# Kernel optimization log

Measured on AMD Instinct MI355X. Metric: run time of the kernel, lower is better.

Reference implementation:

```python
import jax, jax.numpy as jnp
import numpy as np

N_NODES = 50000
N_EDGES = 640000
F = 128          # feat_dims == hidden_dims == out_channels
L = 5            # num_layers of GatedGraphConv


def setup_inputs() -> dict:
    key = jax.random.key(0)
    ks = jax.random.split(key, 9)
    s = 1.0 / np.sqrt(F)
    x = jax.random.normal(ks[0], (N_NODES, F), dtype=jnp.float32)
    edge_index = jax.random.randint(ks[1], (2, N_EDGES), 0, N_NODES, dtype=jnp.int64)
    weight = jax.random.uniform(ks[2], (L, F, F), jnp.float32, -s, s)   # per-layer linear
    w_ih = jax.random.uniform(ks[3], (3 * F, F), jnp.float32, -s, s)     # GRUCell input weights
    w_hh = jax.random.uniform(ks[4], (3 * F, F), jnp.float32, -s, s)     # GRUCell hidden weights
    b_ih = jax.random.uniform(ks[5], (3 * F,), jnp.float32, -s, s)
    b_hh = jax.random.uniform(ks[6], (3 * F,), jnp.float32, -s, s)
    lin_w = jax.random.uniform(ks[7], (1, F), jnp.float32, -s, s)
    lin_b = jax.random.uniform(ks[8], (1,), jnp.float32, -s, s)
    return {"x": x, "edge_index": edge_index, "weight": weight,
            "w_ih": w_ih, "w_hh": w_hh, "b_ih": b_ih, "b_hh": b_hh,
            "lin_w": lin_w, "lin_b": lin_b}


def _gru_cell(m, h, w_ih, w_hh, b_ih, b_hh):
    gi = m @ w_ih.T + b_ih          # [N, 3F]
    gh = h @ w_hh.T + b_hh          # [N, 3F]
    i_r, i_z, i_n = jnp.split(gi, 3, axis=-1)
    h_r, h_z, h_n = jnp.split(gh, 3, axis=-1)
    r = jax.nn.sigmoid(i_r + h_r)
    z = jax.nn.sigmoid(i_z + h_z)
    n = jnp.tanh(i_n + r * h_n)
    return (1.0 - z) * n + z * h


def reference(x, edge_index, weight, w_ih, w_hh, b_ih, b_hh, lin_w, lin_b):
    src = edge_index[0]   # message source (x_j)
    dst = edge_index[1]   # aggregation target
    n_nodes = x.shape[0]
    h = x  # in_channels == out_channels, no padding needed
    for i in range(L):
        m = h @ weight[i]                                   # [N, F]
        agg = jax.ops.segment_sum(m[src], dst, num_segments=n_nodes)  # add-aggregate
        h = _gru_cell(agg, h, w_ih, w_hh, b_ih, b_hh)
    out = jax.nn.relu(h) @ lin_w.T + lin_b                  # [N, 1]
    return out
```

## Files before the change

kernel.cpp:

```cpp
#include <hip/hip_runtime.h>

typedef float f32x4 __attribute__((ext_vector_type(4)));
typedef __bf16 bf16x8 __attribute__((ext_vector_type(8)));
typedef unsigned short u16x8 __attribute__((ext_vector_type(8)));

#define F 128

__device__ __forceinline__ unsigned short bf16_rne(float f) {
  unsigned u = __float_as_uint(f);
  u += 0x7FFFu + ((u >> 16) & 1u);
  return (unsigned short)(u >> 16);
}
__device__ __forceinline__ float bf16f(unsigned short s) {
  return __uint_as_float((unsigned)s << 16);
}


__global__ void split8_kernel(const float* __restrict__ in,
                              unsigned short* __restrict__ hi, unsigned short* __restrict__ lo,
                              int N) {
  int i = blockIdx.x * 256 + threadIdx.x;
  if (i >= N * 16) return;
  int node = i >> 4, f8 = i & 15;
  const float4* p = (const float4*)(in + (size_t)node * F + f8 * 8);
  float4 a = p[0], b = p[1];
  float v[8] = {a.x, a.y, a.z, a.w, b.x, b.y, b.z, b.w};
  u16x8 vh, vl;
#pragma unroll
  for (int e = 0; e < 8; ++e) {
    unsigned short x = bf16_rne(v[e]);
    vh[e] = x;
    vl[e] = bf16_rne(v[e] - bf16f(x));
  }
  size_t o = (size_t)node * F + f8 * 8;
  *(u16x8*)(hi + o) = vh;
  *(u16x8*)(lo + o) = vl;
}

__global__ void prep_w_kernel(const float* __restrict__ W, const float* __restrict__ w_ih,
                              const float* __restrict__ w_hh,
                              unsigned short* __restrict__ Bpack, int L) {
  int idx = blockIdx.x * 256 + threadIdx.x;
  if (idx >= L * 98304) return;
  int e = idx & 7;
  int l = (idx >> 3) & 63;
  int fp = idx >> 9;
  int part = fp % 3;
  int rest = fp / 3;
  int w = rest & 7, g = (rest >> 3) & 1, ks = (rest >> 4) & 3, t = rest >> 6;
  int j = part * 128 + w * 16 + (l & 15);
  int k = ks * 32 + ((l >> 4) & 3) * 8 + e;
  float v;
  if (g == 0) {
    const float* wi = w_ih + (size_t)j * 128;
    const float* wk = W + (size_t)t * 16384 + (size_t)k * 128;
    float acc = 0.f;
#pragma unroll 4
    for (int c = 0; c < 128; ++c) acc = fmaf(wk[c], wi[c], acc);
    v = acc;
  } else {
    v = w_hh[(size_t)j * 128 + k];
  }
  int ff = ((ks * 2 + g) * 8 + w) * 3 + part;
  size_t base = (size_t)t * 196608 + (size_t)ff * 1024 + l * 8 + e;
  unsigned short x = bf16_rne(v);
  Bpack[base] = x;
  Bpack[base + 512] = bf16_rne(v - bf16f(x));
}

__global__ void hist_kernel(const int* __restrict__ ei, int* __restrict__ cnt, int E) {
  int e = blockIdx.x * 256 + threadIdx.x;
  if (e < E) atomicAdd(&cnt[ei[E + e]], 1);
}

__global__ void scan1_kernel(const int* __restrict__ cnt, int* __restrict__ exscan,
                             int* __restrict__ chunk_sums, int N) {
  __shared__ int tmp[256];
  int i = blockIdx.x * 256 + threadIdx.x;
  int v = (i < N) ? cnt[i] : 0;
  tmp[threadIdx.x] = v;
  __syncthreads();
#pragma unroll
  for (int off = 1; off < 256; off <<= 1) {
    int a = (threadIdx.x >= off) ? tmp[threadIdx.x - off] : 0;
    __syncthreads();
    tmp[threadIdx.x] += a;
    __syncthreads();
  }
  if (i < N) exscan[i] = tmp[threadIdx.x] - v;
  if (threadIdx.x == 255) chunk_sums[blockIdx.x] = tmp[255];
}

__global__ void scan2_kernel(int* __restrict__ chunk_sums, int nchunk) {
  __shared__ int tmp[256];
  int v = (threadIdx.x < nchunk) ? chunk_sums[threadIdx.x] : 0;
  tmp[threadIdx.x] = v;
  __syncthreads();
#pragma unroll
  for (int off = 1; off < 256; off <<= 1) {
    int a = (threadIdx.x >= off) ? tmp[threadIdx.x - off] : 0;
    __syncthreads();
    tmp[threadIdx.x] += a;
    __syncthreads();
  }
  if (threadIdx.x < nchunk) chunk_sums[threadIdx.x] = tmp[threadIdx.x] - v;
}

__global__ void finalize_rowptr_kernel(const int* __restrict__ exscan,
                                       const int* __restrict__ chunk_sums,
                                       int* __restrict__ rowptr, int* __restrict__ cursor,
                                       int N, int E) {
  int i = blockIdx.x * 256 + threadIdx.x;
  if (i < N) {
    int v = exscan[i] + chunk_sums[i >> 8];
    rowptr[i] = v;
    cursor[i] = v;
  }
  if (i == N) rowptr[N] = E;
}

__global__ void place_kernel(const int* __restrict__ ei, int* __restrict__ cursor,
                             int* __restrict__ csr_src, int E) {
  int e = blockIdx.x * 256 + threadIdx.x;
  if (e >= E) return;
  int pos = atomicAdd(&cursor[ei[E + e]], 1);
  csr_src[pos] = ei[e];
}

__global__ __launch_bounds__(256) void gather_kernel(
    const unsigned short* __restrict__ hh, const unsigned short* __restrict__ hl,
    const int* __restrict__ rowptr, const int* __restrict__ csr_src,
    unsigned short* __restrict__ shi, unsigned short* __restrict__ slo, int N) {
  int node = blockIdx.x * 4 + (threadIdx.x >> 6);
  if (node >= N) return;
  const int lane = threadIdx.x & 63;
  const int grp = lane >> 4, sub = lane & 15;
  const int par = grp >> 1;
  const unsigned short* base = (grp & 1) ? hl : hh;
  const int beg = rowptr[node], end = rowptr[node + 1];
  float a[8] = {0.f, 0.f, 0.f, 0.f, 0.f, 0.f, 0.f, 0.f};
  int j = beg;
  for (; j + 8 <= end; j += 8) {
    int e0 = csr_src[j + par];
    int e1 = csr_src[j + 2 + par];
    int e2 = csr_src[j + 4 + par];
    int e3 = csr_src[j + 6 + par];
    u16x8 v0 = *(const u16x8*)(base + (size_t)e0 * F + sub * 8);
    u16x8 v1 = *(const u16x8*)(base + (size_t)e1 * F + sub * 8);
    u16x8 v2 = *(const u16x8*)(base + (size_t)e2 * F + sub * 8);
    u16x8 v3 = *(const u16x8*)(base + (size_t)e3 * F + sub * 8);
#pragma unroll
    for (int q = 0; q < 8; ++q)
      a[q] += (bf16f(v0[q]) + bf16f(v1[q])) + (bf16f(v2[q]) + bf16f(v3[q]));
  }
  for (; j + 2 <= end; j += 2) {
    int e0 = csr_src[j + par];
    u16x8 v0 = *(const u16x8*)(base + (size_t)e0 * F + sub * 8);
#pragma unroll
    for (int q = 0; q < 8; ++q) a[q] += bf16f(v0[q]);
  }
  if (j < end && par == 0) {
    int e0 = csr_src[j];
    u16x8 v0 = *(const u16x8*)(base + (size_t)e0 * F + sub * 8);
#pragma unroll
    for (int q = 0; q < 8; ++q) a[q] += bf16f(v0[q]);
  }
#pragma unroll
  for (int q = 0; q < 8; ++q) {
    a[q] += __shfl_xor(a[q], 32, 64);
    a[q] += __shfl_xor(a[q], 16, 64);
  }
  if (grp == 0) {
    u16x8 o;
#pragma unroll
    for (int q = 0; q < 8; ++q) o[q] = bf16_rne(a[q]);
    *(u16x8*)(shi + (size_t)node * F + sub * 8) = o;
  } else if (grp == 1) {
    u16x8 o;
#pragma unroll
    for (int q = 0; q < 8; ++q) {
      unsigned short x = bf16_rne(a[q]);
      o[q] = bf16_rne(a[q] - bf16f(x));
    }
    *(u16x8*)(slo + (size_t)node * F + sub * 8) = o;
  }
}

__device__ __forceinline__ void g2l(const void* g, void* l) {
  __builtin_amdgcn_global_load_lds((const __attribute__((address_space(1))) void*)g,
                                   (__attribute__((address_space(3))) void*)l, 16, 0, 0);
}

#define LOADB(hs, slot)                                                          \
  {                                                                              \
    const unsigned char* bg = Bbase + (size_t)(hs) * 49152;                      \
    _Pragma("unroll") for (int i = 0; i < 6; ++i)                                \
        Bf[slot][i] = *(const bf16x8*)(bg + i * 1024);                           \
  }
#define LOADA(hs, slot)                                                          \
  {                                                                              \
    const int ks_ = (hs) >> 1, g_ = (hs) & 1;                                    \
    const unsigned char* bh = lds + ((g_ * 2) * 4 + ks_) * 4096 + lrow * 64 + kq * 16;      \
    const unsigned char* bl = lds + ((g_ * 2 + 1) * 4 + ks_) * 4096 + lrow * 64 + kq * 16;  \
    _Pragma("unroll") for (int t = 0; t < 4; ++t) {                              \
      Af[slot][t] = *(const bf16x8*)(bh + t * 1024);                             \
      Af[slot][4 + t] = *(const bf16x8*)(bl + t * 1024);                         \
    }                                                                            \
  }
#define DOMFMA(hs, slot)                                                         \
  {                                                                              \
    const int g_ = (hs) & 1;                                                     \
    __builtin_amdgcn_s_setprio(1);                                               \
    _Pragma("unroll") for (int part = 0; part < 3; ++part)                       \
        _Pragma("unroll") for (int t = 0; t < 4; ++t) {                          \
      const int ai = (t * 3 + part) * 2 + g_;                                    \
      acc[ai] = __builtin_amdgcn_mfma_f32_16x16x32_bf16(Af[slot][t], Bf[slot][part * 2], acc[ai], 0, 0, 0);     \
      acc[ai] = __builtin_amdgcn_mfma_f32_16x16x32_bf16(Af[slot][4 + t], Bf[slot][part * 2], acc[ai], 0, 0, 0); \
      acc[ai] = __builtin_amdgcn_mfma_f32_16x16x32_bf16(Af[slot][t], Bf[slot][part * 2 + 1], acc[ai], 0, 0, 0); \
    }                                                                            \
    __builtin_amdgcn_s_setprio(0);                                               \
  }

#define ABSTRIDE 1056

__global__ __launch_bounds__(512, 2) void gemm_gru_kernel(
    const unsigned short* __restrict__ s_hi, const unsigned short* __restrict__ s_lo,
    const unsigned short* h_hi, const unsigned short* h_lo,
    const unsigned short* __restrict__ Bpack,
    const float* __restrict__ bih, const float* __restrict__ bhh,
    unsigned short* h_hi_out, unsigned short* h_lo_out, int N) {
  __shared__ __align__(1024) unsigned char lds[64 * ABSTRIDE];
  const int tid = threadIdx.x, w = tid >> 6, lane = tid & 63;
  const int lrow = lane & 15, kq = lane >> 4;
  const int row0 = blockIdx.x * 64;

  {
    const int arr = w >> 1;
    const unsigned short* ap = (arr == 0) ? s_hi : (arr == 1) ? s_lo : (arr == 2) ? h_hi : h_lo;
#pragma unroll
    for (int i = 0; i < 8; ++i) {
      const int ks = (2 * w + (i >> 2)) & 3;
      int r = row0 + (i & 3) * 16 + (lane >> 2);
      if (r >= N) r = N - 1;
      const unsigned short* g = ap + (size_t)r * F + ks * 32 + (lane & 3) * 8;
      g2l(g, lds + (w * 8 + i) * 1024 + lane * 16);
    }
  }

  f32x4 acc[24];
#pragma unroll
  for (int i = 0; i < 24; ++i) acc[i] = (f32x4){0.f, 0.f, 0.f, 0.f};
  bf16x8 Bf[2][6];
  bf16x8 Af[2][8];

  const unsigned char* Bbase = (const unsigned char*)Bpack + (size_t)w * 6144 + lane * 16;

  asm volatile("s_waitcnt vmcnt(0)" ::: "memory");
  __syncthreads();

  LOADB(0, 0) LOADA(0, 0)
  LOADB(1, 1) LOADA(1, 1) DOMFMA(0, 0)
  LOADB(2, 0) LOADA(2, 0) DOMFMA(1, 1)
  LOADB(3, 1) LOADA(3, 1) DOMFMA(2, 0)
  LOADB(4, 0) LOADA(4, 0) DOMFMA(3, 1)
  LOADB(5, 1) LOADA(5, 1) DOMFMA(4, 0)
  LOADB(6, 0) LOADA(6, 0) DOMFMA(5, 1)
  LOADB(7, 1) LOADA(7, 1) DOMFMA(6, 0)
  DOMFMA(7, 1)

  __syncthreads();

  {
    const int c = w * 16 + lrow;
    const float br = bih[c] + bhh[c];
    const float bz = bih[128 + c] + bhh[128 + c];
    const float bni = bih[256 + c], bnh = bhh[256 + c];
    unsigned char* abp = lds + (size_t)(kq * 4) * ABSTRIDE + c * 8;
#pragma unroll
    for (int t = 0; t < 4; ++t) {
#pragma unroll
      for (int i = 0; i < 4; ++i) {
        const float c1r = acc[(t * 3 + 0) * 2 + 0][i], c2r = acc[(t * 3 + 0) * 2 + 1][i];
        const float c1z = acc[(t * 3 + 1) * 2 + 0][i], c2z = acc[(t * 3 + 1) * 2 + 1][i];
        const float c1n = acc[(t * 3 + 2) * 2 + 0][i], c2n = acc[(t * 3 + 2) * 2 + 1][i];
        const float rr = 1.f / (1.f + __expf(-(c1r + c2r + br)));
        const float zz = 1.f / (1.f + __expf(-(c1z + c2z + bz)));
        const float nn = tanhf(c1n + bni + rr * (c2n + bnh));
        *(float2*)(abp + (size_t)(t * 16 + i) * ABSTRIDE) = make_float2((1.f - zz) * nn, zz);
      }
    }
  }
  __syncthreads();

  {
    const int row = tid >> 3, seg = tid & 7;
    const int r = row0 + row;
    if (r < N) {
      const unsigned char* abp = lds + (size_t)row * ABSTRIDE + seg * 128;
      f32x4 p[8];
#pragma unroll
      for (int k = 0; k < 8; ++k) p[k] = *(const f32x4*)(abp + k * 16);
      const size_t go = (size_t)r * F + seg * 16;
      u16x8 vh0 = *(const u16x8*)(h_hi_out + go);
      u16x8 vh1 = *(const u16x8*)(h_hi_out + go + 8);
      u16x8 vl0 = *(const u16x8*)(h_lo_out + go);
      u16x8 vl1 = *(const u16x8*)(h_lo_out + go + 8);
      u16x8 oh0, oh1, ol0, ol1;
#pragma unroll
      for (int k = 0; k < 4; ++k) {
        float h0 = bf16f(vh0[2 * k]) + bf16f(vl0[2 * k]);
        float h1 = bf16f(vh0[2 * k + 1]) + bf16f(vl0[2 * k + 1]);
        float n0 = p[k].x + p[k].y * h0;
        float n1 = p[k].z + p[k].w * h1;
        unsigned short x0 = bf16_rne(n0), x1 = bf16_rne(n1);
        oh0[2 * k] = x0;
        ol0[2 * k] = bf16_rne(n0 - bf16f(x0));
        oh0[2 * k + 1] = x1;
        ol0[2 * k + 1] = bf16_rne(n1 - bf16f(x1));
      }
#pragma unroll
      for (int k = 0; k < 4; ++k) {
        float h0 = bf16f(vh1[2 * k]) + bf16f(vl1[2 * k]);
        float h1 = bf16f(vh1[2 * k + 1]) + bf16f(vl1[2 * k + 1]);
        float n0 = p[4 + k].x + p[4 + k].y * h0;
        float n1 = p[4 + k].z + p[4 + k].w * h1;
        unsigned short x0 = bf16_rne(n0), x1 = bf16_rne(n1);
        oh1[2 * k] = x0;
        ol1[2 * k] = bf16_rne(n0 - bf16f(x0));
        oh1[2 * k + 1] = x1;
        ol1[2 * k + 1] = bf16_rne(n1 - bf16f(x1));
      }
      *(u16x8*)(h_hi_out + go) = oh0;
      *(u16x8*)(h_hi_out + go + 8) = oh1;
      *(u16x8*)(h_lo_out + go) = ol0;
      *(u16x8*)(h_lo_out + go + 8) = ol1;
    }
  }
}

__global__ void final_kernel(const unsigned* __restrict__ hh, const unsigned* __restrict__ hl,
                             const float* __restrict__ lin_w,
                             const float* __restrict__ lin_b, float* __restrict__ out, int N) {
  int n = blockIdx.x * 4 + (threadIdx.x >> 6);
  if (n >= N) return;
  int d = threadIdx.x & 63;
  size_t o = (size_t)n * 64 + d;
  unsigned wh = hh[o], wl = hl[o];
  float v0 = bf16f((unsigned short)(wh & 0xffff)) + bf16f((unsigned short)(wl & 0xffff));
  float v1 = bf16f((unsigned short)(wh >> 16)) + bf16f((unsigned short)(wl >> 16));
  float sum = fmaxf(v0, 0.f) * lin_w[2 * d] + fmaxf(v1, 0.f) * lin_w[2 * d + 1];
#pragma unroll
  for (int s = 32; s; s >>= 1) sum += __shfl_xor(sum, s, 64);
  if (d == 0) out[n] = sum + lin_b[0];
}

extern "C" void kernel_launch(void* const* d_in, const int* in_sizes, int n_in,
                              void* d_out, int out_size, void* d_ws, size_t ws_size,
                              hipStream_t stream) {
  const float* x     = (const float*)d_in[0];
  const int*   ei    = (const int*)d_in[1];
  const float* W     = (const float*)d_in[2];
  const float* w_ih  = (const float*)d_in[3];
  const float* w_hh  = (const float*)d_in[4];
  const float* b_ih  = (const float*)d_in[5];
  const float* b_hh  = (const float*)d_in[6];
  const float* lin_w = (const float*)d_in[7];
  const float* lin_b = (const float*)d_in[8];

  const int N = in_sizes[0] / F;
  const int E = in_sizes[1] / 2;
  const int L = in_sizes[2] / (F * F);
  const size_t NF = (size_t)N * F;

  char* p = (char*)d_ws;
  unsigned short* h_hi = (unsigned short*)p; p += NF * 2;
  unsigned short* h_lo = (unsigned short*)p; p += NF * 2;
  unsigned short* s_hi = (unsigned short*)p; p += NF * 2;
  unsigned short* s_lo = (unsigned short*)p; p += NF * 2;
  unsigned short* Bpack = (unsigned short*)p; p += (size_t)L * 196608 * 2;
  int* cnt     = (int*)p; p += (size_t)N * 4;
  int* exscan  = (int*)p; p += (size_t)N * 4;
  int* chunk   = (int*)p; p += 256 * 4;
  int* rowptr  = (int*)p; p += ((size_t)N + 1) * 4;
  int* cursor  = (int*)p; p += (size_t)N * 4;
  int* csr_src = (int*)p; p += (size_t)E * 4;

  const int split_blocks = (N * 16 + 255) / 256;
  const int prep_blocks = (L * 98304 + 255) / 256;
  const int edge_blocks = (E + 255) / 256;
  const int nchunk = (N + 255) / 256;
  const int gemm_blocks = (N + 63) / 64;
  const int node4_blocks = (N + 3) / 4;

  split8_kernel<<<split_blocks, 256, 0, stream>>>(x, h_hi, h_lo, N);
  prep_w_kernel<<<prep_blocks, 256, 0, stream>>>(W, w_ih, w_hh, Bpack, L);

  hipMemsetAsync(cnt, 0, (size_t)N * 4, stream);
  hist_kernel<<<edge_blocks, 256, 0, stream>>>(ei, cnt, E);
  scan1_kernel<<<nchunk, 256, 0, stream>>>(cnt, exscan, chunk, N);
  scan2_kernel<<<1, 256, 0, stream>>>(chunk, nchunk);
  finalize_rowptr_kernel<<<(N + 256) / 256, 256, 0, stream>>>(exscan, chunk, rowptr, cursor, N, E);
  place_kernel<<<edge_blocks, 256, 0, stream>>>(ei, cursor, csr_src, E);

  for (int t = 0; t < L; ++t) {
    gather_kernel<<<node4_blocks, 256, 0, stream>>>(
        h_hi, h_lo, rowptr, csr_src, s_hi, s_lo, N);
    gemm_gru_kernel<<<gemm_blocks, 512, 0, stream>>>(
        s_hi, s_lo, h_hi, h_lo, Bpack + (size_t)t * 196608,
        b_ih, b_hh, h_hi, h_lo, N);
  }

  final_kernel<<<node4_blocks, 256, 0, stream>>>(
      (const unsigned*)h_hi, (const unsigned*)h_lo, lin_w, lin_b, (float*)d_out, N);
}
```

Before: 629.8 us.

## Merge r/z accumulators, triple-buffer B fragments, prefetch h before epilogue

The r and z gate accumulators for the s-half and h-half are now summed in a single accumulator, since the GRU only needs their sum. This cuts acc registers from 24 to 16 f32x4. The freed registers go to a third B-fragment buffer, so global B loads are issued two stages ahead of the MFMAs. The h_hi/h_lo reads for the final GRU combine are also hoisted above the gate epilogue so their latency overlaps the transcendental math. The added buffering and the early loads raise live-register pressure around the epilogue.

```diff
diff --git a/kernel.cpp b/kernel.cpp
--- a/kernel.cpp
+++ b/kernel.cpp
@@ -207,16 +207,16 @@
       Af[slot][4 + t] = *(const bf16x8*)(bl + t * 1024);                         \
     }                                                                            \
   }
-#define DOMFMA(hs, slot)                                                         \
+#define DOMFMA(hs, bslot, aslot)                                                 \
   {                                                                              \
     const int g_ = (hs) & 1;                                                     \
     __builtin_amdgcn_s_setprio(1);                                               \
     _Pragma("unroll") for (int part = 0; part < 3; ++part)                       \
         _Pragma("unroll") for (int t = 0; t < 4; ++t) {                          \
-      const int ai = (t * 3 + part) * 2 + g_;                                    \
-      acc[ai] = __builtin_amdgcn_mfma_f32_16x16x32_bf16(Af[slot][t], Bf[slot][part * 2], acc[ai], 0, 0, 0);     \
-      acc[ai] = __builtin_amdgcn_mfma_f32_16x16x32_bf16(Af[slot][4 + t], Bf[slot][part * 2], acc[ai], 0, 0, 0); \
-      acc[ai] = __builtin_amdgcn_mfma_f32_16x16x32_bf16(Af[slot][t], Bf[slot][part * 2 + 1], acc[ai], 0, 0, 0); \
+      const int ai = (part == 2) ? (t * 4 + 2 + g_) : (t * 4 + part);            \
+      acc[ai] = __builtin_amdgcn_mfma_f32_16x16x32_bf16(Af[aslot][t], Bf[bslot][part * 2], acc[ai], 0, 0, 0);     \
+      acc[ai] = __builtin_amdgcn_mfma_f32_16x16x32_bf16(Af[aslot][4 + t], Bf[bslot][part * 2], acc[ai], 0, 0, 0); \
+      acc[ai] = __builtin_amdgcn_mfma_f32_16x16x32_bf16(Af[aslot][t], Bf[bslot][part * 2 + 1], acc[ai], 0, 0, 0); \
     }                                                                            \
     __builtin_amdgcn_s_setprio(0);                                               \
   }
@@ -247,10 +247,10 @@
     }
   }
 
-  f32x4 acc[24];
-#pragma unroll
-  for (int i = 0; i < 24; ++i) acc[i] = (f32x4){0.f, 0.f, 0.f, 0.f};
-  bf16x8 Bf[2][6];
+  f32x4 acc[16];
+#pragma unroll
+  for (int i = 0; i < 16; ++i) acc[i] = (f32x4){0.f, 0.f, 0.f, 0.f};
+  bf16x8 Bf[3][6];
   bf16x8 Af[2][8];
 
   const unsigned char* Bbase = (const unsigned char*)Bpack + (size_t)w * 6144 + lane * 16;
@@ -258,17 +258,25 @@
   asm volatile("s_waitcnt vmcnt(0)" ::: "memory");
   __syncthreads();
 
-  LOADB(0, 0) LOADA(0, 0)
-  LOADB(1, 1) LOADA(1, 1) DOMFMA(0, 0)
-  LOADB(2, 0) LOADA(2, 0) DOMFMA(1, 1)
-  LOADB(3, 1) LOADA(3, 1) DOMFMA(2, 0)
-  LOADB(4, 0) LOADA(4, 0) DOMFMA(3, 1)
-  LOADB(5, 1) LOADA(5, 1) DOMFMA(4, 0)
-  LOADB(6, 0) LOADA(6, 0) DOMFMA(5, 1)
-  LOADB(7, 1) LOADA(7, 1) DOMFMA(6, 0)
-  DOMFMA(7, 1)
+  LOADB(0, 0) LOADA(0, 0) LOADB(1, 1) LOADB(2, 2)
+  LOADA(1, 1) DOMFMA(0, 0, 0)
+  LOADB(3, 0) LOADA(2, 0) DOMFMA(1, 1, 1)
+  LOADB(4, 1) LOADA(3, 1) DOMFMA(2, 2, 0)
+  LOADB(5, 2) LOADA(4, 0) DOMFMA(3, 0, 1)
+  LOADB(6, 0) LOADA(5, 1) DOMFMA(4, 1, 0)
+  LOADB(7, 1) LOADA(6, 0) DOMFMA(5, 2, 1)
+  LOADA(7, 1) DOMFMA(6, 0, 0)
+  DOMFMA(7, 1, 1)
 
   __syncthreads();
+
+  const int row2 = tid >> 3, seg2 = tid & 7;
+  const int r2 = row0 + row2;
+  const size_t go2 = (size_t)(r2 < N ? r2 : 0) * F + seg2 * 16;
+  u16x8 vh0 = *(const u16x8*)(h_hi_out + go2);
+  u16x8 vh1 = *(const u16x8*)(h_hi_out + go2 + 8);
+  u16x8 vl0 = *(const u16x8*)(h_lo_out + go2);
+  u16x8 vl1 = *(const u16x8*)(h_lo_out + go2 + 8);
 
   {
     const int c = w * 16 + lrow;
@@ -280,11 +288,11 @@
     for (int t = 0; t < 4; ++t) {
 #pragma unroll
       for (int i = 0; i < 4; ++i) {
-        const float c1r = acc[(t * 3 + 0) * 2 + 0][i], c2r = acc[(t * 3 + 0) * 2 + 1][i];
-        const float c1z = acc[(t * 3 + 1) * 2 + 0][i], c2z = acc[(t * 3 + 1) * 2 + 1][i];
-        const float c1n = acc[(t * 3 + 2) * 2 + 0][i], c2n = acc[(t * 3 + 2) * 2 + 1][i];
-        const float rr = 1.f / (1.f + __expf(-(c1r + c2r + br)));
-        const float zz = 1.f / (1.f + __expf(-(c1z + c2z + bz)));
+        const float cr = acc[t * 4 + 0][i];
+        const float cz = acc[t * 4 + 1][i];
+        const float c1n = acc[t * 4 + 2][i], c2n = acc[t * 4 + 3][i];
+        const float rr = 1.f / (1.f + __expf(-(cr + br)));
+        const float zz = 1.f / (1.f + __expf(-(cz + bz)));
         const float nn = tanhf(c1n + bni + rr * (c2n + bnh));
         *(float2*)(abp + (size_t)(t * 16 + i) * ABSTRIDE) = make_float2((1.f - zz) * nn, zz);
       }
@@ -292,49 +300,40 @@
   }
   __syncthreads();
 
-  {
-    const int row = tid >> 3, seg = tid & 7;
-    const int r = row0 + row;
-    if (r < N) {
-      const unsigned char* abp = lds + (size_t)row * ABSTRIDE + seg * 128;
-      f32x4 p[8];
-#pragma unroll
-      for (int k = 0; k < 8; ++k) p[k] = *(const f32x4*)(abp + k * 16);
-      const size_t go = (size_t)r * F + seg * 16;
-      u16x8 vh0 = *(const u16x8*)(h_hi_out + go);
-      u16x8 vh1 = *(const u16x8*)(h_hi_out + go + 8);
-      u16x8 vl0 = *(const u16x8*)(h_lo_out + go);
-      u16x8 vl1 = *(const u16x8*)(h_lo_out + go + 8);
-      u16x8 oh0, oh1, ol0, ol1;
-#pragma unroll
-      for (int k = 0; k < 4; ++k) {
-        float h0 = bf16f(vh0[2 * k]) + bf16f(vl0[2 * k]);
-        float h1 = bf16f(vh0[2 * k + 1]) + bf16f(vl0[2 * k + 1]);
-        float n0 = p[k].x + p[k].y * h0;
-        float n1 = p[k].z + p[k].w * h1;
-        unsigned short x0 = bf16_rne(n0), x1 = bf16_rne(n1);
-        oh0[2 * k] = x0;
-        ol0[2 * k] = bf16_rne(n0 - bf16f(x0));
-        oh0[2 * k + 1] = x1;
-        ol0[2 * k + 1] = bf16_rne(n1 - bf16f(x1));
-      }
-#pragma unroll
-      for (int k = 0; k < 4; ++k) {
-        float h0 = bf16f(vh1[2 * k]) + bf16f(vl1[2 * k]);
-        float h1 = bf16f(vh1[2 * k + 1]) + bf16f(vl1[2 * k + 1]);
-        float n0 = p[4 + k].x + p[4 + k].y * h0;
-        float n1 = p[4 + k].z + p[4 + k].w * h1;
-        unsigned short x0 = bf16_rne(n0), x1 = bf16_rne(n1);
-        oh1[2 * k] = x0;
-        ol1[2 * k] = bf16_rne(n0 - bf16f(x0));
-        oh1[2 * k + 1] = x1;
-        ol1[2 * k + 1] = bf16_rne(n1 - bf16f(x1));
-      }
-      *(u16x8*)(h_hi_out + go) = oh0;
-      *(u16x8*)(h_hi_out + go + 8) = oh1;
-      *(u16x8*)(h_lo_out + go) = ol0;
-      *(u16x8*)(h_lo_out + go + 8) = ol1;
+  if (r2 < N) {
+    const unsigned char* abp = lds + (size_t)row2 * ABSTRIDE + seg2 * 128;
+    f32x4 p[8];
+#pragma unroll
+    for (int k = 0; k < 8; ++k) p[k] = *(const f32x4*)(abp + k * 16);
+    u16x8 oh0, oh1, ol0, ol1;
+#pragma unroll
+    for (int k = 0; k < 4; ++k) {
+      float h0 = bf16f(vh0[2 * k]) + bf16f(vl0[2 * k]);
+      float h1 = bf16f(vh0[2 * k + 1]) + bf16f(vl0[2 * k + 1]);
+      float n0 = p[k].x + p[k].y * h0;
+      float n1 = p[k].z + p[k].w * h1;
+      unsigned short x0 = bf16_rne(n0), x1 = bf16_rne(n1);
+      oh0[2 * k] = x0;
+      ol0[2 * k] = bf16_rne(n0 - bf16f(x0));
+      oh0[2 * k + 1] = x1;
+      ol0[2 * k + 1] = bf16_rne(n1 - bf16f(x1));
     }
+#pragma unroll
+    for (int k = 0; k < 4; ++k) {
+      float h0 = bf16f(vh1[2 * k]) + bf16f(vl1[2 * k]);
+      float h1 = bf16f(vh1[2 * k + 1]) + bf16f(vl1[2 * k + 1]);
+      float n0 = p[4 + k].x + p[4 + k].y * h0;
+      float n1 = p[4 + k].z + p[4 + k].w * h1;
+      unsigned short x0 = bf16_rne(n0), x1 = bf16_rne(n1);
+      oh1[2 * k] = x0;
+      ol1[2 * k] = bf16_rne(n0 - bf16f(x0));
+      oh1[2 * k + 1] = x1;
+      ol1[2 * k + 1] = bf16_rne(n1 - bf16f(x1));
+    }
+    *(u16x8*)(h_hi_out + go2) = oh0;
+    *(u16x8*)(h_hi_out + go2 + 8) = oh1;
+    *(u16x8*)(h_lo_out + go2) = ol0;
+    *(u16x8*)(h_lo_out + go2 + 8) = ol1;
   }
 }
 
```

After: 640.1 us. Within noise of the previous version (+1.6%).
